# Kernel tuning notes

Hardware: AMD Instinct MI355X
Metric: run time of the kernel (lower is better)

The kernel has to match this reference:

```python
import jax, jax.numpy as jnp
import numpy as np

B, S, D, H = 2, 2048, 1024, 16
HD = D // H  # head_dim = 64

def setup_inputs() -> dict:
    key = jax.random.key(0)
    ks = jax.random.split(key, 11)
    s = 1.0 / np.sqrt(D)
    return {
        "query_input": jax.random.normal(ks[0], (B, S, D), jnp.float32),
        "key_input":   jax.random.normal(ks[1], (B, S, D), jnp.float32),
        "value_input": jax.random.normal(ks[2], (B, S, D), jnp.float32),
        "Wq": jax.random.normal(ks[3], (D, D), jnp.float32) * s,
        "bq": jnp.zeros((D,), jnp.float32),
        "Wk": jax.random.normal(ks[4], (D, D), jnp.float32) * s,
        "bk": jnp.zeros((D,), jnp.float32),
        "Wv": jax.random.normal(ks[5], (D, D), jnp.float32) * s,
        "bv": jnp.zeros((D,), jnp.float32),
        "Wo": jax.random.normal(ks[6], (D, D), jnp.float32) * s,
        "bo": jnp.zeros((D,), jnp.float32),
    }

def _split_heads(x):
    b, s, _ = x.shape
    return x.reshape(b, s, H, HD).transpose(0, 2, 1, 3)  # [B,H,S,HD]

def reference(query_input, key_input, value_input, Wq, bq, Wk, bk, Wv, bv, Wo, bo):
    q = _split_heads(query_input @ Wq + bq)
    k = _split_heads(key_input @ Wk + bk)
    v = _split_heads(value_input @ Wv + bv)
    scores = jnp.einsum('bhqd,bhkd->bhqk', q, k) / jnp.sqrt(jnp.float32(HD))
    attn = jax.nn.softmax(scores, axis=-1)
    out = jnp.einsum('bhqk,bhkd->bhqd', attn, v)
    out = out.transpose(0, 2, 1, 3).reshape(query_input.shape[0], -1, H * HD)
    return out @ Wo + bo
```

## Files before the change

kernel.cpp:

```cpp
#include <hip/hip_runtime.h>
#include <hip/hip_bf16.h>
#include <math.h>

#define B_  2
#define S_  2048
#define D_  1024
#define H_  16
#define HD_ 64

typedef __bf16  bf16x8   __attribute__((ext_vector_type(8)));
typedef float   floatx4  __attribute__((ext_vector_type(4)));
typedef float   floatx16 __attribute__((ext_vector_type(16)));

#define MFMA16(a, b, c) __builtin_amdgcn_mfma_f32_16x16x32_bf16((a), (b), (c), 0, 0, 0)
#define MFMA32(a, b, c) __builtin_amdgcn_mfma_f32_32x32x16_bf16((a), (b), (c), 0, 0, 0)

__device__ __forceinline__ void load_lds16(const void* g, void* l) {
    __builtin_amdgcn_global_load_lds(
        (const __attribute__((address_space(1))) unsigned int*)g,
        (__attribute__((address_space(3))) unsigned int*)l, 16, 0, 0);
}

__device__ __forceinline__ unsigned pk_bf16(float a, float b) {
    unsigned r;
    asm("v_cvt_pk_bf16_f32 %0, %1, %2" : "=v"(r) : "v"(a), "v"(b));
    return r;
}

__global__ __launch_bounds__(256) void cast3_bf16_k(
    const float* __restrict__ x0, const float* __restrict__ x1, const float* __restrict__ x2,
    __hip_bfloat16* __restrict__ o0, __hip_bfloat16* __restrict__ o1, __hip_bfloat16* __restrict__ o2)
{
    const int z = blockIdx.y;
    const float* src = (z == 0) ? x0 : (z == 1) ? x1 : x2;
    __hip_bfloat16* dst = (z == 0) ? o0 : (z == 1) ? o1 : o2;
    const int i = blockIdx.x * 256 + threadIdx.x;
    const float4* s4 = (const float4*)src;
    const float4 a = s4[2 * i + 0];
    const float4 b = s4[2 * i + 1];
    union { __hip_bfloat16 h[8]; uint4 v; } p;
    p.h[0] = __float2bfloat16(a.x); p.h[1] = __float2bfloat16(a.y);
    p.h[2] = __float2bfloat16(a.z); p.h[3] = __float2bfloat16(a.w);
    p.h[4] = __float2bfloat16(b.x); p.h[5] = __float2bfloat16(b.y);
    p.h[6] = __float2bfloat16(b.z); p.h[7] = __float2bfloat16(b.w);
    ((uint4*)dst)[i] = p.v;
}

__global__ __launch_bounds__(256) void transpose4_cast_k(
    const float* __restrict__ W0, const float* __restrict__ W1,
    const float* __restrict__ W2, const float* __restrict__ W3,
    __hip_bfloat16* __restrict__ T0, __hip_bfloat16* __restrict__ T1,
    __hip_bfloat16* __restrict__ T2, __hip_bfloat16* __restrict__ T3)
{
    const int z = blockIdx.z;
    const float* W = (z == 0) ? W0 : (z == 1) ? W1 : (z == 2) ? W2 : W3;
    __hip_bfloat16* Wt = (z == 0) ? T0 : (z == 1) ? T1 : (z == 2) ? T2 : T3;

    __shared__ float T[64][65];
    const int t  = threadIdx.x;
    const int n0 = blockIdx.x * 64, k0 = blockIdx.y * 64;
    #pragma unroll
    for (int i = 0; i < 4; ++i) {
        const int u = t + i * 256;
        const int r = u >> 4, c4 = (u & 15) * 4;
        const float4 v = *(const float4*)(W + (size_t)(k0 + r) * D_ + n0 + c4);
        T[r][c4 + 0] = v.x; T[r][c4 + 1] = v.y; T[r][c4 + 2] = v.z; T[r][c4 + 3] = v.w;
    }
    __syncthreads();
    #pragma unroll
    for (int i = 0; i < 4; ++i) {
        const int u = t + i * 256;
        const int n = u >> 4, c4 = (u & 15) * 4;
        union { __hip_bfloat16 h[4]; uint2 v; } p;
        #pragma unroll
        for (int j = 0; j < 4; ++j) p.h[j] = __float2bfloat16(T[c4 + j][n]);
        *(uint2*)(Wt + (size_t)(n0 + n) * D_ + k0 + c4) = p.v;
    }
}

__global__ __launch_bounds__(256) void gemm_qkv_k(
    const __hip_bfloat16* __restrict__ xq, const __hip_bfloat16* __restrict__ xk,
    const __hip_bfloat16* __restrict__ xv,
    const __hip_bfloat16* __restrict__ WqT, const __hip_bfloat16* __restrict__ WkT,
    const __hip_bfloat16* __restrict__ WvT,
    const float* __restrict__ bq, const float* __restrict__ bk, const float* __restrict__ bv,
    __hip_bfloat16* __restrict__ Qh, __hip_bfloat16* __restrict__ Kh,
    __hip_bfloat16* __restrict__ Vt)
{
    constexpr int K = 1024;
    __shared__ __align__(16) short As0[128][32], As1[128][32];
    __shared__ __align__(16) short Bs0[128][32], Bs1[128][32];

    const int z = blockIdx.z;
    const __hip_bfloat16* A  = (z == 0) ? xq  : (z == 1) ? xk  : xv;
    const __hip_bfloat16* Bt = (z == 0) ? WqT : (z == 1) ? WkT : WvT;
    const float* bias        = (z == 0) ? bq  : (z == 1) ? bk  : bv;

    const int t    = threadIdx.x;
    const int lane = t & 63, w = t >> 6;
    const int quad = lane >> 4, l16 = lane & 15;
    const int m0   = blockIdx.x * 128, n0 = blockIdx.y * 128;
    const int wm   = (w >> 1) * 64,    wn = (w & 1) * 64;

    floatx4 acc[4][4] = {};

    auto stage = [&](int k0, short (*As)[32], short (*Bs)[32]) {
        #pragma unroll
        for (int i = 0; i < 2; ++i) {
            const int c = t + i * 256;
            const int m = c >> 2, kq = (c ^ (m >> 1)) & 3;
            load_lds16(A + (size_t)(m0 + m) * K + k0 + kq * 8, &As[0][0] + c * 8);
        }
        #pragma unroll
        for (int i = 0; i < 2; ++i) {
            const int c = t + i * 256;
            const int n = c >> 2, kq = (c ^ (n >> 1)) & 3;
            load_lds16(Bt + (size_t)(n0 + n) * K + k0 + kq * 8, &Bs[0][0] + c * 8);
        }
    };

    auto compute = [&](short (*As)[32], short (*Bs)[32]) {
        bf16x8 af[4], bfr[4];
        #pragma unroll
        for (int mt = 0; mt < 4; ++mt) {
            const int r = wm + mt * 16 + l16;
            af[mt]  = *(const bf16x8*)&As[r][((quad ^ (r >> 1)) & 3) * 8];
        }
        #pragma unroll
        for (int nt = 0; nt < 4; ++nt) {
            const int n = wn + nt * 16 + l16;
            bfr[nt] = *(const bf16x8*)&Bs[n][((quad ^ (n >> 1)) & 3) * 8];
        }
        #pragma unroll
        for (int mt = 0; mt < 4; ++mt)
            #pragma unroll
            for (int nt = 0; nt < 4; ++nt)
                acc[mt][nt] = MFMA16(af[mt], bfr[nt], acc[mt][nt]);
    };

    stage(0, As0, Bs0);
    for (int k0 = 0; k0 < K; k0 += 64) {
        __syncthreads();
        stage(k0 + 32, As1, Bs1);
        compute(As0, Bs0);
        __syncthreads();
        if (k0 + 64 < K) stage(k0 + 64, As0, Bs0);
        compute(As1, Bs1);
    }

    if (z != 2) {
        const float oscale = (z == 0) ? 0.125f : 1.0f;
        __hip_bfloat16* outp = (z == 0) ? Qh : Kh;
        #pragma unroll
        for (int mt = 0; mt < 4; ++mt)
            #pragma unroll
            for (int nt = 0; nt < 4; ++nt) {
                const int gn = n0 + wn + nt * 16 + l16;
                const float bi = bias[gn];
                #pragma unroll
                for (int r = 0; r < 4; ++r) {
                    const int gm = m0 + wm + mt * 16 + quad * 4 + r;
                    const float v = (acc[mt][nt][r] + bi) * oscale;
                    outp[(((size_t)(gm >> 11) * H_ + (gn >> 6)) * S_ + (gm & 2047)) * 64 + (gn & 63)] =
                        __float2bfloat16(v);
                }
            }
    } else {
        #pragma unroll
        for (int mt = 0; mt < 4; ++mt)
            #pragma unroll
            for (int nt = 0; nt < 4; ++nt) {
                const int gn = n0 + wn + nt * 16 + l16;
                const float bi = bias[gn];
                const int gm0 = m0 + wm + mt * 16 + quad * 4;
                union { __hip_bfloat16 h[4]; uint2 u; } pk;
                #pragma unroll
                for (int r = 0; r < 4; ++r) pk.h[r] = __float2bfloat16(acc[mt][nt][r] + bi);
                *(uint2*)(Vt + (((size_t)(gm0 >> 11) * H_ + (gn >> 6)) * 64 + (gn & 63)) * S_ +
                          (gm0 & 2047)) = pk.u;
            }
    }
}

__global__ __launch_bounds__(256) void gemm_oproj_k(
    const __hip_bfloat16* __restrict__ A, const __hip_bfloat16* __restrict__ Bt,
    const float* __restrict__ bias, float* __restrict__ out)
{
    constexpr int K = 1024, N = 1024;
    __shared__ __align__(16) short As0[128][32], As1[128][32];
    __shared__ __align__(16) short Bs0[64][32],  Bs1[64][32];

    const int t    = threadIdx.x;
    const int lane = t & 63, w = t >> 6;
    const int quad = lane >> 4, l16 = lane & 15;
    const int m0   = blockIdx.x * 128, n0 = blockIdx.y * 64;
    const int wm   = (w >> 1) * 64,    wn = (w & 1) * 32;

    floatx4 acc[4][2] = {};

    auto stage = [&](int k0, short (*As)[32], short (*Bs)[32]) {
        #pragma unroll
        for (int i = 0; i < 2; ++i) {
            const int c = t + i * 256;
            const int m = c >> 2, kq = (c ^ (m >> 1)) & 3;
            load_lds16(A + (size_t)(m0 + m) * K + k0 + kq * 8, &As[0][0] + c * 8);
        }
        {
            const int c = t;
            const int n = c >> 2, kq = (c ^ (n >> 1)) & 3;
            load_lds16(Bt + (size_t)(n0 + n) * K + k0 + kq * 8, &Bs[0][0] + c * 8);
        }
    };

    auto compute = [&](short (*As)[32], short (*Bs)[32]) {
        bf16x8 af[4], bfr[2];
        #pragma unroll
        for (int mt = 0; mt < 4; ++mt) {
            const int r = wm + mt * 16 + l16;
            af[mt]  = *(const bf16x8*)&As[r][((quad ^ (r >> 1)) & 3) * 8];
        }
        #pragma unroll
        for (int nt = 0; nt < 2; ++nt) {
            const int n = wn + nt * 16 + l16;
            bfr[nt] = *(const bf16x8*)&Bs[n][((quad ^ (n >> 1)) & 3) * 8];
        }
        #pragma unroll
        for (int mt = 0; mt < 4; ++mt)
            #pragma unroll
            for (int nt = 0; nt < 2; ++nt)
                acc[mt][nt] = MFMA16(af[mt], bfr[nt], acc[mt][nt]);
    };

    stage(0, As0, Bs0);
    for (int k0 = 0; k0 < K; k0 += 64) {
        __syncthreads();
        stage(k0 + 32, As1, Bs1);
        compute(As0, Bs0);
        __syncthreads();
        if (k0 + 64 < K) stage(k0 + 64, As0, Bs0);
        compute(As1, Bs1);
    }

    #pragma unroll
    for (int mt = 0; mt < 4; ++mt)
        #pragma unroll
        for (int nt = 0; nt < 2; ++nt) {
            const int gn = n0 + wn + nt * 16 + l16;
            const float bi = bias[gn];
            #pragma unroll
            for (int r = 0; r < 4; ++r) {
                const int gm = m0 + wm + mt * 16 + quad * 4 + r;
                out[(size_t)gm * N + gn] = acc[mt][nt][r] + bi;
            }
        }
}

__global__ __launch_bounds__(256) void attn_mfma_k(
    const __hip_bfloat16* __restrict__ Qh, const __hip_bfloat16* __restrict__ Kh,
    const __hip_bfloat16* __restrict__ Vt, __hip_bfloat16* __restrict__ Ctx)
{
    __shared__ __align__(16) short Ks0[64][64], Ks1[64][64];
    __shared__ __align__(16) short Vs0[64][64], Vs1[64][64];

    const int t    = threadIdx.x;
    const int lane = t & 63, w = t >> 6;
    const int l32  = lane & 31, hi = lane >> 5;
    const int b = blockIdx.z, h = blockIdx.x;
    const size_t bh = (size_t)b * H_ + h;
    const int q0 = blockIdx.y * 128;

    bf16x8 qf[4];
    {
        const __hip_bfloat16* qb = Qh + (bh * S_ + q0 + w * 32 + l32) * 64 + hi * 8;
        #pragma unroll
        for (int ks = 0; ks < 4; ++ks) qf[ks] = *(const bf16x8*)(qb + ks * 16);
    }

    floatx16 oacc[2] = {};
    float ls = 0.f;

    auto stage = [&](int kt, short (*Ks)[64], short (*Vs)[64]) {
        #pragma unroll
        for (int i = 0; i < 2; ++i) {
            const int c = t + i * 256;
            const int p = c >> 3, kq = (c ^ p) & 7;
            load_lds16(Kh + (bh * S_ + kt * 64 + p) * 64 + kq * 8, &Ks[0][0] + c * 8);
            load_lds16(Vt + (bh * 64 + p) * S_ + kt * 64 + kq * 8, &Vs[0][0] + c * 8);
        }
    };

    auto mkfrags = [&](const float (&e)[16], bf16x8* fr) {
        #pragma unroll
        for (int k2 = 0; k2 < 2; ++k2) {
            unsigned y0 = pk_bf16(e[8 * k2 + 0], e[8 * k2 + 1]);
            unsigned y1 = pk_bf16(e[8 * k2 + 2], e[8 * k2 + 3]);
            unsigned y2 = pk_bf16(e[8 * k2 + 4], e[8 * k2 + 5]);
            unsigned y3 = pk_bf16(e[8 * k2 + 6], e[8 * k2 + 7]);
            asm volatile("v_permlane32_swap_b32 %0, %1" : "+v"(y0), "+v"(y2));
            asm volatile("v_permlane32_swap_b32 %0, %1" : "+v"(y1), "+v"(y3));
            union { unsigned u[4]; bf16x8 v; } pq;
            pq.u[0] = y0; pq.u[1] = y1; pq.u[2] = y2; pq.u[3] = y3;
            fr[k2] = pq.v;
        }
    };

    auto compute = [&](short (*Ks)[64], short (*Vs)[64]) {
        floatx16 sacc[2] = {};
        __builtin_amdgcn_s_setprio(1);
        #pragma unroll
        for (int a = 0; a < 2; ++a) {
            const int row = a * 32 + l32;
            #pragma unroll
            for (int ks = 0; ks < 4; ++ks) {
                const bf16x8 kf =
                    *(const bf16x8*)&Ks[row][(((ks * 2 + hi) ^ row) & 7) * 8];
                sacc[a] = MFMA32(kf, qf[ks], sacc[a]);
            }
        }
        __builtin_amdgcn_s_setprio(0);

        float e0[16], e1[16];
        #pragma unroll
        for (int r = 0; r < 16; ++r) { e0[r] = __expf(sacc[0][r]); ls += e0[r]; }
        #pragma unroll
        for (int r = 0; r < 16; ++r) { e1[r] = __expf(sacc[1][r]); ls += e1[r]; }

        bf16x8 pa[4];
        mkfrags(e0, &pa[0]);
        mkfrags(e1, &pa[2]);

        __builtin_amdgcn_s_setprio(1);
        #pragma unroll
        for (int nt = 0; nt < 2; ++nt) {
            const int row = nt * 32 + l32;
            #pragma unroll
            for (int f = 0; f < 4; ++f) {
                const bf16x8 vf =
                    *(const bf16x8*)&Vs[row][(((f * 2 + hi) ^ row) & 7) * 8];
                oacc[nt] = MFMA32(pa[f], vf, oacc[nt]);
            }
        }
        __builtin_amdgcn_s_setprio(0);
    };

    stage(0, Ks0, Vs0);
    for (int kt = 0; kt < S_ / 64; kt += 2) {
        __syncthreads();
        stage(kt + 1, Ks1, Vs1);
        compute(Ks0, Vs0);
        __syncthreads();
        if (kt + 2 < S_ / 64) stage(kt + 2, Ks0, Vs0);
        compute(Ks1, Vs1);
    }

    ls += __shfl_xor(ls, 32, 64);
    const float inv = 1.0f / ls;
    float den[16];
    #pragma unroll
    for (int r = 0; r < 16; ++r)
        den[r] = __shfl(inv, (r & 3) + 8 * (r >> 2) + 4 * hi, 64);

    #pragma unroll
    for (int nt = 0; nt < 2; ++nt)
        #pragma unroll
        for (int r = 0; r < 16; ++r) {
            const int qrow = q0 + w * 32 + (r & 3) + 8 * (r >> 2) + 4 * hi;
            const int hd   = nt * 32 + l32;
            Ctx[((size_t)b * S_ + qrow) * D_ + h * 64 + hd] =
                __float2bfloat16(oacc[nt][r] * den[r]);
        }
}

extern "C" void kernel_launch(void* const* d_in, const int* in_sizes, int n_in,
                              void* d_out, int out_size, void* d_ws, size_t ws_size,
                              hipStream_t stream)
{
    const float* xq = (const float*)d_in[0];
    const float* xk = (const float*)d_in[1];
    const float* xv = (const float*)d_in[2];
    const float* Wq = (const float*)d_in[3];
    const float* bq = (const float*)d_in[4];
    const float* Wk = (const float*)d_in[5];
    const float* bk = (const float*)d_in[6];
    const float* Wv = (const float*)d_in[7];
    const float* bv = (const float*)d_in[8];
    const float* Wo = (const float*)d_in[9];
    const float* bo = (const float*)d_in[10];
    float* out = (float*)d_out;

    const size_t n = (size_t)B_ * S_ * D_;
    char* p = (char*)d_ws;
    __hip_bfloat16* xqb = (__hip_bfloat16*)p;            p += n * 2;
    __hip_bfloat16* xkb = (__hip_bfloat16*)p;            p += n * 2;
    __hip_bfloat16* xvb = (__hip_bfloat16*)p;            p += n * 2;
    __hip_bfloat16* WqT = (__hip_bfloat16*)p;            p += (size_t)D_ * D_ * 2;
    __hip_bfloat16* WkT = (__hip_bfloat16*)p;            p += (size_t)D_ * D_ * 2;
    __hip_bfloat16* WvT = (__hip_bfloat16*)p;            p += (size_t)D_ * D_ * 2;
    __hip_bfloat16* WoT = (__hip_bfloat16*)p;            p += (size_t)D_ * D_ * 2;
    __hip_bfloat16* Qh  = (__hip_bfloat16*)p;            p += n * 2;
    __hip_bfloat16* Kh  = (__hip_bfloat16*)p;            p += n * 2;
    __hip_bfloat16* Vth = (__hip_bfloat16*)p;            p += n * 2;
    __hip_bfloat16* Ctx = (__hip_bfloat16*)p;            p += n * 2;

    cast3_bf16_k<<<dim3((int)(n / 8 / 256), 3), dim3(256), 0, stream>>>(
        xq, xk, xv, xqb, xkb, xvb);
    transpose4_cast_k<<<dim3(16, 16, 4), dim3(256), 0, stream>>>(
        Wq, Wk, Wv, Wo, WqT, WkT, WvT, WoT);

    gemm_qkv_k<<<dim3((B_ * S_) / 128, D_ / 128, 3), dim3(256), 0, stream>>>(
        xqb, xkb, xvb, WqT, WkT, WvT, bq, bk, bv, Qh, Kh, Vth);

    attn_mfma_k<<<dim3(H_, S_ / 128, B_), dim3(256), 0, stream>>>(Qh, Kh, Vth, Ctx);

    gemm_oproj_k<<<dim3((B_ * S_) / 128, D_ / 64), dim3(256), 0, stream>>>(
        Ctx, WoT, bo, out);
}
```

Measured before the change: 224.3 us.

## Split attention KV range across two wave groups and use hardware exp2

The attention block grows to 512 threads. Each half of the waves processes half of the key/value sequence with its own double-buffered LDS tiles, and the partial outputs and row sums are merged through shared memory at the end. Separately, the softmax scale now folds log2(e) into the Q projection so the kernel can call v_exp_f32 directly instead of __expf. The split doubles the waves available to hide latency per query tile, at the cost of extra LDS, a reduction step and larger blocks that may lower occupancy.

Measured after the change: 220.3 us (median of 2 runs). No clear change (-1.8%).

```diff
diff --git a/kernel.cpp b/kernel.cpp
--- a/kernel.cpp
+++ b/kernel.cpp
@@ -24,6 +24,12 @@
 __device__ __forceinline__ unsigned pk_bf16(float a, float b) {
     unsigned r;
     asm("v_cvt_pk_bf16_f32 %0, %1, %2" : "=v"(r) : "v"(a), "v"(b));
+    return r;
+}
+
+__device__ __forceinline__ float exp2_hw(float x) {
+    float r;
+    asm("v_exp_f32 %0, %1" : "=v"(r) : "v"(x));
     return r;
 }
 
@@ -149,7 +155,7 @@
     }
 
     if (z != 2) {
-        const float oscale = (z == 0) ? 0.125f : 1.0f;
+        const float oscale = (z == 0) ? 0.125f * 1.44269504088896f : 1.0f;
         __hip_bfloat16* outp = (z == 0) ? Qh : Kh;
         #pragma unroll
         for (int mt = 0; mt < 4; ++mt)
@@ -255,23 +261,30 @@
         }
 }
 
-__global__ __launch_bounds__(256) void attn_mfma_k(
+union AttnSmem {
+    struct { short K0[2][64][64], K1[2][64][64], V0[2][64][64], V1[2][64][64]; } s;
+    struct { float O[4][64][33]; float L[4][32]; } c;
+};
+
+__global__ __launch_bounds__(512) void attn_mfma_k(
     const __hip_bfloat16* __restrict__ Qh, const __hip_bfloat16* __restrict__ Kh,
     const __hip_bfloat16* __restrict__ Vt, __hip_bfloat16* __restrict__ Ctx)
 {
-    __shared__ __align__(16) short Ks0[64][64], Ks1[64][64];
-    __shared__ __align__(16) short Vs0[64][64], Vs1[64][64];
+    __shared__ __align__(16) AttnSmem sm;
 
     const int t    = threadIdx.x;
     const int lane = t & 63, w = t >> 6;
     const int l32  = lane & 31, hi = lane >> 5;
+    const int wq   = w & 3, half = w >> 2;
+    const int ht   = t & 255;
     const int b = blockIdx.z, h = blockIdx.x;
     const size_t bh = (size_t)b * H_ + h;
     const int q0 = blockIdx.y * 128;
+    const int kvbase = half * 16;
 
     bf16x8 qf[4];
     {
-        const __hip_bfloat16* qb = Qh + (bh * S_ + q0 + w * 32 + l32) * 64 + hi * 8;
+        const __hip_bfloat16* qb = Qh + (bh * S_ + q0 + wq * 32 + l32) * 64 + hi * 8;
         #pragma unroll
         for (int ks = 0; ks < 4; ++ks) qf[ks] = *(const bf16x8*)(qb + ks * 16);
     }
@@ -282,7 +295,7 @@
     auto stage = [&](int kt, short (*Ks)[64], short (*Vs)[64]) {
         #pragma unroll
         for (int i = 0; i < 2; ++i) {
-            const int c = t + i * 256;
+            const int c = ht + i * 256;
             const int p = c >> 3, kq = (c ^ p) & 7;
             load_lds16(Kh + (bh * S_ + kt * 64 + p) * 64 + kq * 8, &Ks[0][0] + c * 8);
             load_lds16(Vt + (bh * 64 + p) * S_ + kt * 64 + kq * 8, &Vs[0][0] + c * 8);
@@ -321,9 +334,9 @@
 
         float e0[16], e1[16];
         #pragma unroll
-        for (int r = 0; r < 16; ++r) { e0[r] = __expf(sacc[0][r]); ls += e0[r]; }
-        #pragma unroll
-        for (int r = 0; r < 16; ++r) { e1[r] = __expf(sacc[1][r]); ls += e1[r]; }
+        for (int r = 0; r < 16; ++r) { e0[r] = exp2_hw(sacc[0][r]); ls += e0[r]; }
+        #pragma unroll
+        for (int r = 0; r < 16; ++r) { e1[r] = exp2_hw(sacc[1][r]); ls += e1[r]; }
 
         bf16x8 pa[4];
         mkfrags(e0, &pa[0]);
@@ -343,32 +356,47 @@
         __builtin_amdgcn_s_setprio(0);
     };
 
-    stage(0, Ks0, Vs0);
-    for (int kt = 0; kt < S_ / 64; kt += 2) {
-        __syncthreads();
-        stage(kt + 1, Ks1, Vs1);
-        compute(Ks0, Vs0);
-        __syncthreads();
-        if (kt + 2 < S_ / 64) stage(kt + 2, Ks0, Vs0);
-        compute(Ks1, Vs1);
+    stage(kvbase, sm.s.K0[half], sm.s.V0[half]);
+    for (int kt = 0; kt < 16; kt += 2) {
+        __syncthreads();
+        stage(kvbase + kt + 1, sm.s.K1[half], sm.s.V1[half]);
+        compute(sm.s.K0[half], sm.s.V0[half]);
+        __syncthreads();
+        if (kt + 2 < 16) stage(kvbase + kt + 2, sm.s.K0[half], sm.s.V0[half]);
+        compute(sm.s.K1[half], sm.s.V1[half]);
     }
 
     ls += __shfl_xor(ls, 32, 64);
-    const float inv = 1.0f / ls;
-    float den[16];
-    #pragma unroll
-    for (int r = 0; r < 16; ++r)
-        den[r] = __shfl(inv, (r & 3) + 8 * (r >> 2) + 4 * hi, 64);
-
-    #pragma unroll
-    for (int nt = 0; nt < 2; ++nt)
-        #pragma unroll
-        for (int r = 0; r < 16; ++r) {
-            const int qrow = q0 + w * 32 + (r & 3) + 8 * (r >> 2) + 4 * hi;
-            const int hd   = nt * 32 + l32;
-            Ctx[((size_t)b * S_ + qrow) * D_ + h * 64 + hd] =
-                __float2bfloat16(oacc[nt][r] * den[r]);
-        }
+
+    __syncthreads();
+    if (half == 1) {
+        #pragma unroll
+        for (int nt = 0; nt < 2; ++nt)
+            #pragma unroll
+            for (int r = 0; r < 16; ++r)
+                sm.c.O[wq][lane][nt * 16 + r] = oacc[nt][r];
+        if (hi == 0) sm.c.L[wq][l32] = ls;
+    }
+    __syncthreads();
+    if (half == 0) {
+        ls += sm.c.L[wq][l32];
+        const float inv = 1.0f / ls;
+        float den[16];
+        #pragma unroll
+        for (int r = 0; r < 16; ++r)
+            den[r] = __shfl(inv, (r & 3) + 8 * (r >> 2) + 4 * hi, 64);
+
+        #pragma unroll
+        for (int nt = 0; nt < 2; ++nt)
+            #pragma unroll
+            for (int r = 0; r < 16; ++r) {
+                const int qrow = q0 + wq * 32 + (r & 3) + 8 * (r >> 2) + 4 * hi;
+                const int hd   = nt * 32 + l32;
+                const float o  = oacc[nt][r] + sm.c.O[wq][lane][nt * 16 + r];
+                Ctx[((size_t)b * S_ + qrow) * D_ + h * 64 + hd] =
+                    __float2bfloat16(o * den[r]);
+            }
+    }
 }
 
 extern "C" void kernel_launch(void* const* d_in, const int* in_sizes, int n_in,
@@ -410,7 +438,7 @@
     gemm_qkv_k<<<dim3((B_ * S_) / 128, D_ / 128, 3), dim3(256), 0, stream>>>(
         xqb, xkb, xvb, WqT, WkT, WvT, bq, bk, bv, Qh, Kh, Vth);
 
-    attn_mfma_k<<<dim3(H_, S_ / 128, B_), dim3(256), 0, stream>>>(Qh, Kh, Vth, Ctx);
+    attn_mfma_k<<<dim3(H_, S_ / 128, B_), dim3(512), 0, stream>>>(Qh, Kh, Vth, Ctx);
 
     gemm_oproj_k<<<dim3((B_ * S_) / 128, D_ / 64), dim3(256), 0, stream>>>(
         Ctx, WoT, bo, out);
```
